# Performance work log

Measured on AMD Instinct MI355X. Metric: run time of the kernel, lower is better.

## Reference

```python
import jax, jax.numpy as jnp
import numpy as np

MAX_WORDS = 256  # = batch['labels'].shape[1]


def _align(hidden, word_ids, max_words):
    """Batched segment-mean: (B,S,D) subtoken states -> (B,max_words,D) word states.
    Equivalent to align_subtokens_to_words applied per sample (word_ids all valid)."""
    B, S, D = hidden.shape
    seg = (word_ids.astype(jnp.int32) + jnp.arange(B, dtype=jnp.int32)[:, None] * max_words).reshape(-1)
    sums = jax.ops.segment_sum(hidden.reshape(-1, D), seg, num_segments=B * max_words)
    cnts = jax.ops.segment_sum(jnp.ones((B * S,), hidden.dtype), seg, num_segments=B * max_words)
    out = jnp.where(cnts[:, None] > 0, sums / jnp.maximum(cnts, 1.0)[:, None], 0.0)
    return out.reshape(B, max_words, D)


def setup_inputs() -> dict:
    key = jax.random.key(0)
    ks = jax.random.split(key, 8)
    B, S, D, W = 64, 512, 768, MAX_WORDS
    h_hing_sub = jax.random.normal(ks[0], (B, S, D), dtype=jnp.float32)
    h_rob_sub = jax.random.normal(ks[1], (B, S, D), dtype=jnp.float32)
    hing_word_ids = jnp.sort(jax.random.randint(ks[2], (B, S), 0, W), axis=-1).astype(jnp.int32)
    rob_word_ids = jnp.sort(jax.random.randint(ks[3], (B, S), 0, W), axis=-1).astype(jnp.int32)
    num_words = jax.random.randint(ks[4], (B,), 1, W).astype(jnp.int32)
    router_w1 = jax.random.normal(ks[5], (2 * D, 256), dtype=jnp.float32) * (1.0 / np.sqrt(2 * D))
    router_b1 = jnp.zeros((256,), jnp.float32)
    router_w2 = jax.random.normal(ks[6], (256, 1), dtype=jnp.float32) * (1.0 / 16.0)
    router_b2 = jnp.zeros((1,), jnp.float32)
    head_w = jax.random.normal(ks[7], (D, 7), dtype=jnp.float32) * (1.0 / np.sqrt(D))
    head_b = jnp.zeros((7,), jnp.float32)
    return {
        'h_hing_sub': h_hing_sub, 'h_rob_sub': h_rob_sub,
        'hing_word_ids': hing_word_ids, 'rob_word_ids': rob_word_ids,
        'num_words': num_words,
        'router_w1': router_w1, 'router_b1': router_b1,
        'router_w2': router_w2, 'router_b2': router_b2,
        'head_w': head_w, 'head_b': head_b,
    }


def reference(h_hing_sub, h_rob_sub, hing_word_ids, rob_word_ids, num_words,
              router_w1, router_b1, router_w2, router_b2, head_w, head_b):
    W = MAX_WORDS
    # scatter-mean subtokens -> words (the dominant custom-kernel op)
    h_hing = _align(h_hing_sub, hing_word_ids, W)   # (B, W, 768)
    h_rob = _align(h_rob_sub, rob_word_ids, W)      # (B, W, 768)
    # token-level MLP router on concatenated word states (router_input='both')
    router_in = jnp.concatenate([h_hing, h_rob], axis=-1)             # (B, W, 1536)
    hdn = jax.nn.relu(jnp.einsum('bwd,dh->bwh', router_in, router_w1) + router_b1)
    alpha = jax.nn.sigmoid(jnp.einsum('bwh,ho->bwo', hdn, router_w2) + router_b2)  # (B, W, 1)
    blended = alpha * h_hing + (1.0 - alpha) * h_rob                  # (B, W, 768)
    logits = jnp.einsum('bwd,dl->bwl', blended, head_w) + head_b      # (B, W, num_labels)
    l2_disagreement = jnp.linalg.norm(h_hing - h_rob, axis=-1)        # (B, W)
    return logits, alpha.squeeze(-1), l2_disagreement
```

## Files before the change

kernel.cpp:

```cpp
#include <hip/hip_runtime.h>
#include <hip/hip_bf16.h>
#include <math.h>

#define BATCH 64
#define SEQ   512
#define DIM   768
#define NW    256
#define NT    (BATCH * NW)
#define KDIM  1536
#define HID   256
#define NL    7

#define BM  32
#define BK  64
#define BKP 72
#define NKT (KDIM / BK)

typedef __bf16 bf16_t;
typedef bf16_t bf16x8 __attribute__((ext_vector_type(8)));
typedef float  f32x4  __attribute__((ext_vector_type(4)));

__global__ __launch_bounds__(256) void convert_w1_kernel(
    const float* __restrict__ w1, bf16_t* __restrict__ w1t)
{
    int idx = blockIdx.x * 256 + threadIdx.x;
    int kk = idx & 63;
    int n  = (idx >> 6) & 255;
    int kc = idx >> 14;
    w1t[idx] = (bf16_t)w1[(kc * BK + kk) * HID + n];
}

__device__ __forceinline__ int lower_bound_512(const int* __restrict__ a, int v)
{
    int lo = 0, hi = SEQ;
    while (lo < hi) { int m = (lo + hi) >> 1; if (a[m] < v) lo = m + 1; else hi = m; }
    return lo;
}

__global__ __launch_bounds__(256) void align_kernel(
    const float* __restrict__ hh, const float* __restrict__ hr,
    const int* __restrict__ idh, const int* __restrict__ idr,
    bf16_t* __restrict__ X)
{
    int blk = blockIdx.x;
    int b = blk >> 8;
    int w = blk & 255;
    int tid = threadIdx.x;

    __shared__ int rng[4];
    if (tid == 0) {
        const int* ids = idh + b * SEQ;
        rng[0] = lower_bound_512(ids, w);
        rng[1] = lower_bound_512(ids, w + 1);
    } else if (tid == 64) {
        const int* ids = idr + b * SEQ;
        rng[2] = lower_bound_512(ids, w);
        rng[3] = lower_bound_512(ids, w + 1);
    }
    __syncthreads();
    int loH = rng[0], hiH = rng[1], loR = rng[2], hiR = rng[3];
    float invH = (hiH > loH) ? 1.0f / (float)(hiH - loH) : 0.0f;
    float invR = (hiR > loR) ? 1.0f / (float)(hiR - loR) : 0.0f;

    size_t base = (size_t)b * SEQ * DIM;
    bf16_t* xrow = X + (size_t)blk * KDIM;

    #pragma unroll
    for (int j = 0; j < 3; j++) {
        int d = tid + j * 256;
        float sh = 0.f, sr = 0.f;
        for (int s = loH; s < hiH; s++) sh += hh[base + (size_t)s * DIM + d];
        for (int s = loR; s < hiR; s++) sr += hr[base + (size_t)s * DIM + d];
        xrow[d]       = (bf16_t)(sh * invH);
        xrow[DIM + d] = (bf16_t)(sr * invR);
    }
}

__global__ __launch_bounds__(256) void gemm_fused_kernel(
    const bf16_t* __restrict__ X, const bf16_t* __restrict__ w1t,
    const float* __restrict__ b1, const float* __restrict__ w2,
    const float* __restrict__ b2, const float* __restrict__ hw,
    const float* __restrict__ hb, float* __restrict__ out)
{
    __shared__ __align__(16) bf16_t Xs[BM][BKP];
    __shared__ __align__(16) bf16_t Ws[HID][BKP];
    __shared__ float alpha_acc[BM];
    __shared__ float alpha_s[BM];

    int tid   = threadIdx.x;
    int lane  = tid & 63;
    int wv    = tid >> 6;
    int row16 = lane & 15;
    int quad  = lane >> 4;
    int blk   = blockIdx.x;
    int tok0  = blk * BM;

    f32x4 acc[2][4];
    #pragma unroll
    for (int mi = 0; mi < 2; mi++)
        #pragma unroll
        for (int ni = 0; ni < 4; ni++)
            acc[mi][ni] = (f32x4){0.f, 0.f, 0.f, 0.f};

    int xr = tid >> 3;
    int xc = tid & 7;

    for (int kc = 0; kc < NKT; kc++) {
        {
            const uint4* src = (const uint4*)(X + (size_t)(tok0 + xr) * KDIM + kc * BK + xc * 8);
            *(uint4*)(&Xs[xr][xc * 8]) = *src;
        }
        {
            const uint4* srcb = (const uint4*)(w1t + (size_t)kc * (HID * BK));
            #pragma unroll
            for (int i = 0; i < 8; i++) {
                int cidx = tid + i * 256;
                int n = cidx >> 3;
                int c = cidx & 7;
                *(uint4*)(&Ws[n][c * 8]) = srcb[cidx];
            }
        }
        __syncthreads();
        #pragma unroll
        for (int kk2 = 0; kk2 < 2; kk2++) {
            bf16x8 af[2], bfg[4];
            #pragma unroll
            for (int mi = 0; mi < 2; mi++)
                af[mi] = *(const bf16x8*)(&Xs[mi * 16 + row16][kk2 * 32 + quad * 8]);
            #pragma unroll
            for (int ni = 0; ni < 4; ni++)
                bfg[ni] = *(const bf16x8*)(&Ws[wv * 64 + ni * 16 + row16][kk2 * 32 + quad * 8]);
            #pragma unroll
            for (int mi = 0; mi < 2; mi++)
                #pragma unroll
                for (int ni = 0; ni < 4; ni++)
                    acc[mi][ni] = __builtin_amdgcn_mfma_f32_16x16x32_bf16(
                        af[mi], bfg[ni], acc[mi][ni], 0, 0, 0);
        }
        __syncthreads();
    }

    float w2v[4], b1v[4];
    #pragma unroll
    for (int ni = 0; ni < 4; ni++) {
        int col = wv * 64 + ni * 16 + row16;
        w2v[ni] = w2[col];
        b1v[ni] = b1[col];
    }
    if (tid < BM) alpha_acc[tid] = 0.f;
    __syncthreads();

    #pragma unroll
    for (int mi = 0; mi < 2; mi++) {
        #pragma unroll
        for (int r = 0; r < 4; r++) {
            float p = 0.f;
            #pragma unroll
            for (int ni = 0; ni < 4; ni++) {
                float v = acc[mi][ni][r] + b1v[ni];
                v = v > 0.f ? v : 0.f;
                p += v * w2v[ni];
            }
            p += __shfl_xor(p, 1);
            p += __shfl_xor(p, 2);
            p += __shfl_xor(p, 4);
            p += __shfl_xor(p, 8);
            if (row16 == 0) {
                int rowl = mi * 16 + quad * 4 + r;
                atomicAdd(&alpha_acc[rowl], p);
            }
        }
    }
    __syncthreads();
    if (tid < BM) {
        float a = 1.f / (1.f + expf(-(alpha_acc[tid] + b2[0])));
        alpha_s[tid] = a;
        out[(size_t)NT * NL + tok0 + tid] = a;
    }
    __syncthreads();

    float* out_logits = out;
    float* out_l2 = out + (size_t)NT * NL + NT;

    #pragma unroll
    for (int i = 0; i < 8; i++) {
        int m = wv * 8 + i;
        int tok = tok0 + m;
        float a = alpha_s[m];
        const bf16_t* xrow = X + (size_t)tok * KDIM;
        float lg[NL] = {0.f, 0.f, 0.f, 0.f, 0.f, 0.f, 0.f};
        float l2p = 0.f;
        #pragma unroll
        for (int j = 0; j < 12; j++) {
            int d = lane + j * 64;
            float hhv = (float)xrow[d];
            float hrv = (float)xrow[DIM + d];
            float bl = a * hhv + (1.f - a) * hrv;
            float df = hhv - hrv;
            l2p += df * df;
            const float* hwd = hw + d * NL;
            #pragma unroll
            for (int l = 0; l < NL; l++) lg[l] += bl * hwd[l];
        }
        #pragma unroll
        for (int off = 1; off < 64; off <<= 1) {
            #pragma unroll
            for (int l = 0; l < NL; l++) lg[l] += __shfl_xor(lg[l], off);
            l2p += __shfl_xor(l2p, off);
        }
        if (lane < NL)       out_logits[(size_t)tok * NL + lane] = lg[lane] + hb[lane];
        else if (lane == NL) out_l2[tok] = sqrtf(l2p);
    }
}

extern "C" void kernel_launch(void* const* d_in, const int* in_sizes, int n_in,
                              void* d_out, int out_size, void* d_ws, size_t ws_size,
                              hipStream_t stream)
{
    const float* hh  = (const float*)d_in[0];
    const float* hr  = (const float*)d_in[1];
    const int*   idh = (const int*)d_in[2];
    const int*   idr = (const int*)d_in[3];
    const float* w1  = (const float*)d_in[5];
    const float* b1  = (const float*)d_in[6];
    const float* w2  = (const float*)d_in[7];
    const float* b2  = (const float*)d_in[8];
    const float* hw  = (const float*)d_in[9];
    const float* hb  = (const float*)d_in[10];
    float* out = (float*)d_out;

    bf16_t* X   = (bf16_t*)d_ws;
    bf16_t* w1t = X + (size_t)NT * KDIM;

    convert_w1_kernel<<<(NKT * HID * BK) / 256, 256, 0, stream>>>(w1, w1t);
    align_kernel<<<NT, 256, 0, stream>>>(hh, hr, idh, idr, X);
    gemm_fused_kernel<<<NT / BM, 256, 0, stream>>>(X, w1t, b1, w2, b2, hw, hb, out);
}
```

Baseline: 316.8 us.

## Restructure align to one wave per token, split blend out, tile w1 conversion

The align kernel now gives each wave one word token and uses float4 loads, so a block covers four tokens and the binary searches are spread over 16 threads. The blend/logits/L2 epilogue moves out of the GEMM into its own kernel with vectorized bf16x4 and head-weight loads, one wave per token. The w1 conversion now transposes through an LDS tile so global reads are coalesced. The cost is one extra launch and a second read of X, and the conversion now runs on only 24 blocks.

```diff
diff --git a/kernel.cpp b/kernel.cpp
--- a/kernel.cpp
+++ b/kernel.cpp
@@ -17,17 +17,33 @@
 #define NKT (KDIM / BK)
 
 typedef __bf16 bf16_t;
+typedef bf16_t bf16x4 __attribute__((ext_vector_type(4)));
 typedef bf16_t bf16x8 __attribute__((ext_vector_type(8)));
 typedef float  f32x4  __attribute__((ext_vector_type(4)));
 
 __global__ __launch_bounds__(256) void convert_w1_kernel(
     const float* __restrict__ w1, bf16_t* __restrict__ w1t)
 {
-    int idx = blockIdx.x * 256 + threadIdx.x;
-    int kk = idx & 63;
-    int n  = (idx >> 6) & 255;
-    int kc = idx >> 14;
-    w1t[idx] = (bf16_t)w1[(kc * BK + kk) * HID + n];
+    __shared__ float tile[64 * 257];
+    int tid = threadIdx.x;
+    int kc  = blockIdx.x;
+
+    for (int k = 0; k < 64; k++)
+        tile[k * 257 + tid] = w1[(size_t)(kc * 64 + k) * HID + tid];
+    __syncthreads();
+
+    bf16_t* dst = w1t + (size_t)kc * (HID * BK);
+    #pragma unroll
+    for (int i = 0; i < 8; i++) {
+        int ch = tid + i * 256;
+        int n  = ch >> 3;
+        int c  = ch & 7;
+        bf16x8 v;
+        #pragma unroll
+        for (int j = 0; j < 8; j++)
+            v[j] = (bf16_t)tile[(c * 8 + j) * 257 + n];
+        *(bf16x8*)(dst + n * BK + c * 8) = v;
+    }
 }
 
 __device__ __forceinline__ int lower_bound_512(const int* __restrict__ a, int v)
@@ -42,58 +58,74 @@
     const int* __restrict__ idh, const int* __restrict__ idr,
     bf16_t* __restrict__ X)
 {
-    int blk = blockIdx.x;
-    int b = blk >> 8;
-    int w = blk & 255;
-    int tid = threadIdx.x;
-
-    __shared__ int rng[4];
-    if (tid == 0) {
-        const int* ids = idh + b * SEQ;
-        rng[0] = lower_bound_512(ids, w);
-        rng[1] = lower_bound_512(ids, w + 1);
-    } else if (tid == 64) {
-        const int* ids = idr + b * SEQ;
-        rng[2] = lower_bound_512(ids, w);
-        rng[3] = lower_bound_512(ids, w + 1);
-    }
-    __syncthreads();
-    int loH = rng[0], hiH = rng[1], loR = rng[2], hiR = rng[3];
+    __shared__ int rngS[16];
+    int tid  = threadIdx.x;
+    int lane = tid & 63;
+    int wv   = tid >> 6;
+
+    if (tid < 16) {
+        int tsub  = tid >> 2;
+        int which = (tid >> 1) & 1;
+        int bound = tid & 1;
+        int tok   = blockIdx.x * 4 + tsub;
+        int b     = tok >> 8;
+        int w     = tok & 255;
+        const int* ids = (which ? idr : idh) + b * SEQ;
+        rngS[tid] = lower_bound_512(ids, w + bound);
+    }
+    __syncthreads();
+
+    int tok = blockIdx.x * 4 + wv;
+    int b   = tok >> 8;
+    int loH = rngS[wv * 4 + 0], hiH = rngS[wv * 4 + 1];
+    int loR = rngS[wv * 4 + 2], hiR = rngS[wv * 4 + 3];
+
+    const f32x4* baseH = (const f32x4*)(hh + (size_t)b * SEQ * DIM);
+    const f32x4* baseR = (const f32x4*)(hr + (size_t)b * SEQ * DIM);
+
+    f32x4 aH0 = {0,0,0,0}, aH1 = {0,0,0,0}, aH2 = {0,0,0,0};
+    f32x4 aR0 = {0,0,0,0}, aR1 = {0,0,0,0}, aR2 = {0,0,0,0};
+
+    for (int s = loH; s < hiH; s++) {
+        const f32x4* row = baseH + (size_t)s * (DIM / 4);
+        aH0 += row[lane]; aH1 += row[lane + 64]; aH2 += row[lane + 128];
+    }
+    for (int s = loR; s < hiR; s++) {
+        const f32x4* row = baseR + (size_t)s * (DIM / 4);
+        aR0 += row[lane]; aR1 += row[lane + 64]; aR2 += row[lane + 128];
+    }
+
     float invH = (hiH > loH) ? 1.0f / (float)(hiH - loH) : 0.0f;
     float invR = (hiR > loR) ? 1.0f / (float)(hiR - loR) : 0.0f;
 
-    size_t base = (size_t)b * SEQ * DIM;
-    bf16_t* xrow = X + (size_t)blk * KDIM;
-
-    #pragma unroll
-    for (int j = 0; j < 3; j++) {
-        int d = tid + j * 256;
-        float sh = 0.f, sr = 0.f;
-        for (int s = loH; s < hiH; s++) sh += hh[base + (size_t)s * DIM + d];
-        for (int s = loR; s < hiR; s++) sr += hr[base + (size_t)s * DIM + d];
-        xrow[d]       = (bf16_t)(sh * invH);
-        xrow[DIM + d] = (bf16_t)(sr * invR);
-    }
-}
-
-__global__ __launch_bounds__(256) void gemm_fused_kernel(
+    bf16_t* xrow = X + (size_t)tok * KDIM;
+    f32x4 accs[6] = {aH0, aH1, aH2, aR0, aR1, aR2};
+    #pragma unroll
+    for (int c = 0; c < 6; c++) {
+        float inv = (c < 3) ? invH : invR;
+        int   d0  = (c < 3) ? (lane + 64 * c) * 4 : DIM + (lane + 64 * (c - 3)) * 4;
+        bf16x4 o;
+        #pragma unroll
+        for (int e = 0; e < 4; e++) o[e] = (bf16_t)(accs[c][e] * inv);
+        *(bf16x4*)(xrow + d0) = o;
+    }
+}
+
+__global__ __launch_bounds__(256) void gemm_alpha_kernel(
     const bf16_t* __restrict__ X, const bf16_t* __restrict__ w1t,
     const float* __restrict__ b1, const float* __restrict__ w2,
-    const float* __restrict__ b2, const float* __restrict__ hw,
-    const float* __restrict__ hb, float* __restrict__ out)
+    const float* __restrict__ b2, float* __restrict__ out)
 {
     __shared__ __align__(16) bf16_t Xs[BM][BKP];
     __shared__ __align__(16) bf16_t Ws[HID][BKP];
     __shared__ float alpha_acc[BM];
-    __shared__ float alpha_s[BM];
 
     int tid   = threadIdx.x;
     int lane  = tid & 63;
     int wv    = tid >> 6;
     int row16 = lane & 15;
     int quad  = lane >> 4;
-    int blk   = blockIdx.x;
-    int tok0  = blk * BM;
+    int tok0  = blockIdx.x * BM;
 
     f32x4 acc[2][4];
     #pragma unroll
@@ -115,9 +147,7 @@
             #pragma unroll
             for (int i = 0; i < 8; i++) {
                 int cidx = tid + i * 256;
-                int n = cidx >> 3;
-                int c = cidx & 7;
-                *(uint4*)(&Ws[n][c * 8]) = srcb[cidx];
+                *(uint4*)(&Ws[cidx >> 3][(cidx & 7) * 8]) = srcb[cidx];
             }
         }
         __syncthreads();
@@ -165,52 +195,68 @@
             p += __shfl_xor(p, 2);
             p += __shfl_xor(p, 4);
             p += __shfl_xor(p, 8);
-            if (row16 == 0) {
-                int rowl = mi * 16 + quad * 4 + r;
-                atomicAdd(&alpha_acc[rowl], p);
-            }
+            if (row16 == 0)
+                atomicAdd(&alpha_acc[mi * 16 + quad * 4 + r], p);
         }
     }
     __syncthreads();
     if (tid < BM) {
         float a = 1.f / (1.f + expf(-(alpha_acc[tid] + b2[0])));
-        alpha_s[tid] = a;
         out[(size_t)NT * NL + tok0 + tid] = a;
     }
-    __syncthreads();
-
-    float* out_logits = out;
-    float* out_l2 = out + (size_t)NT * NL + NT;
-
-    #pragma unroll
-    for (int i = 0; i < 8; i++) {
-        int m = wv * 8 + i;
-        int tok = tok0 + m;
-        float a = alpha_s[m];
-        const bf16_t* xrow = X + (size_t)tok * KDIM;
-        float lg[NL] = {0.f, 0.f, 0.f, 0.f, 0.f, 0.f, 0.f};
-        float l2p = 0.f;
-        #pragma unroll
-        for (int j = 0; j < 12; j++) {
-            int d = lane + j * 64;
-            float hhv = (float)xrow[d];
-            float hrv = (float)xrow[DIM + d];
-            float bl = a * hhv + (1.f - a) * hrv;
-            float df = hhv - hrv;
-            l2p += df * df;
-            const float* hwd = hw + d * NL;
-            #pragma unroll
-            for (int l = 0; l < NL; l++) lg[l] += bl * hwd[l];
-        }
-        #pragma unroll
-        for (int off = 1; off < 64; off <<= 1) {
-            #pragma unroll
-            for (int l = 0; l < NL; l++) lg[l] += __shfl_xor(lg[l], off);
-            l2p += __shfl_xor(l2p, off);
-        }
-        if (lane < NL)       out_logits[(size_t)tok * NL + lane] = lg[lane] + hb[lane];
-        else if (lane == NL) out_l2[tok] = sqrtf(l2p);
-    }
+}
+
+__global__ __launch_bounds__(256) void blend_kernel(
+    const bf16_t* __restrict__ X, const float* __restrict__ hw,
+    const float* __restrict__ hb, float* __restrict__ out)
+{
+    int tid  = threadIdx.x;
+    int lane = tid & 63;
+    int wv   = tid >> 6;
+    int tok  = blockIdx.x * 4 + wv;
+
+    const float* alpha = out + (size_t)NT * NL;
+    float a = alpha[tok];
+    const bf16_t* xrow = X + (size_t)tok * KDIM;
+
+    float lg[NL] = {0.f, 0.f, 0.f, 0.f, 0.f, 0.f, 0.f};
+    float l2 = 0.f;
+
+    #pragma unroll
+    for (int j = 0; j < 3; j++) {
+        int d0 = (lane + 64 * j) * 4;
+        bf16x4 hp = *(const bf16x4*)(xrow + d0);
+        bf16x4 rp = *(const bf16x4*)(xrow + DIM + d0);
+        const f32x4* hwv = (const f32x4*)(hw + (size_t)d0 * NL);
+        f32x4 wv4[7];
+        #pragma unroll
+        for (int q = 0; q < 7; q++) wv4[q] = hwv[q];
+        #pragma unroll
+        for (int e = 0; e < 4; e++) {
+            float hhv = (float)hp[e];
+            float hrv = (float)rp[e];
+            float bl  = a * hhv + (1.f - a) * hrv;
+            float df  = hhv - hrv;
+            l2 += df * df;
+            #pragma unroll
+            for (int l = 0; l < NL; l++) {
+                int idx = e * NL + l;
+                lg[l] += bl * wv4[idx >> 2][idx & 3];
+            }
+        }
+    }
+
+    #pragma unroll
+    for (int off = 1; off < 64; off <<= 1) {
+        #pragma unroll
+        for (int l = 0; l < NL; l++) lg[l] += __shfl_xor(lg[l], off);
+        l2 += __shfl_xor(l2, off);
+    }
+
+    if (lane < NL)
+        out[(size_t)tok * NL + lane] = lg[lane] + hb[lane];
+    else if (lane == NL)
+        out[(size_t)NT * NL + NT + tok] = sqrtf(l2);
 }
 
 extern "C" void kernel_launch(void* const* d_in, const int* in_sizes, int n_in,
@@ -232,7 +278,8 @@
     bf16_t* X   = (bf16_t*)d_ws;
     bf16_t* w1t = X + (size_t)NT * KDIM;
 
-    convert_w1_kernel<<<(NKT * HID * BK) / 256, 256, 0, stream>>>(w1, w1t);
-    align_kernel<<<NT, 256, 0, stream>>>(hh, hr, idh, idr, X);
-    gemm_fused_kernel<<<NT / BM, 256, 0, stream>>>(X, w1t, b1, w2, b2, hw, hb, out);
-}
+    convert_w1_kernel<<<NKT, 256, 0, stream>>>(w1, w1t);
+    align_kernel<<<NT / 4, 256, 0, stream>>>(hh, hr, idh, idr, X);
+    gemm_alpha_kernel<<<NT / BM, 256, 0, stream>>>(X, w1t, b1, w2, b2, out);
+    blend_kernel<<<NT / 4, 256, 0, stream>>>(X, hw, hb, out);
+}
```

Measured after the change: 297.4 us. -6.1%, faster.
